# Kernel tuning notes

Hardware: AMD Instinct MI355X
Metric: run time of the kernel (lower is better)

Reference implementation:

```python
import jax, jax.numpy as jnp
import numpy as np

B, T, C = 64, 2048, 32
OUT_T = 2048

def setup_inputs() -> dict:
    key = jax.random.key(0)
    k1, k2 = jax.random.split(key)
    X = jax.random.normal(k1, (B, T, C), dtype=jnp.float32)
    # small init so deformations are modest displacements, like a trained locnet
    W_loc = jax.random.normal(k2, (T * C, OUT_T), dtype=jnp.float32) * 1e-3
    b_loc = jnp.zeros((OUT_T,), dtype=jnp.float32)
    return {"X": X, "W_loc": W_loc, "b_loc": b_loc}

def reference(X, W_loc, b_loc):
    b, t, c = X.shape
    out_t = W_loc.shape[1]
    # localization net: flatten + dense -> per-output-point displacement (B, OUT_T)
    deformation = X.reshape(b, t * c) @ W_loc + b_loc
    # sampling grid: linspace(0, T-1, OUT_T), shared across batch, shifted by deformation
    grid = jnp.linspace(0.0, jnp.float32(t - 1), out_t)  # (OUT_T,)
    x = grid[None, :] + deformation                       # (B, OUT_T) float sample coords
    # linear interpolation with clamped integer neighbors
    x0 = jnp.floor(x).astype(jnp.int32)
    x1 = x0 + 1
    x0c = jnp.clip(x0, 0, t - 1)
    x1c = jnp.clip(x1, 0, t - 1)
    batch_idx = jnp.arange(b)[:, None]                    # (B, 1)
    v0 = X[batch_idx, x0c]                                # (B, OUT_T, C) gather along T
    v1 = X[batch_idx, x1c]                                # (B, OUT_T, C)
    # weights use the CLIPPED coords cast back to float (faithful to original)
    w0 = (x1c.astype(x.dtype) - x)[..., None]             # (B, OUT_T, 1)
    w1 = (x - x0c.astype(x.dtype))[..., None]
    return w0 * v0 + w1 * v1                              # (B, OUT_T, C)
```

## Files before the change

### kernel.cpp

```cpp
#include <hip/hip_runtime.h>
#include <hip/hip_bf16.h>
#include <stdint.h>

constexpr int BATCH = 64;
constexpr int T     = 2048;
constexpr int CCH   = 32;
constexpr int OUT_T = 2048;
constexpr int K     = T * CCH;
constexpr int N     = OUT_T;

constexpr int TN     = 64;
constexpr int NBN    = N / TN;
constexpr int KSPLIT = 32;
constexpr int CK     = K / KSPLIT;
constexpr int BK     = 32;
constexpr int NS     = CK / BK;
constexpr int NWG    = NBN * KSPLIT;

typedef __attribute__((ext_vector_type(8))) short short8;
typedef __attribute__((ext_vector_type(4))) float f32x4;

__device__ __forceinline__ void split2t(float a, float b, unsigned& hpk, unsigned& lpk) {
  unsigned ua = __float_as_uint(a), ub = __float_as_uint(b);
  hpk = (ua >> 16) | (ub & 0xFFFF0000u);
  float la = a - __uint_as_float(ua & 0xFFFF0000u);
  float lb = b - __uint_as_float(ub & 0xFFFF0000u);
  __hip_bfloat162 l2 = __float22bfloat162_rn(make_float2(la, lb));
  __builtin_memcpy(&lpk, &l2, 4);
}

__global__ __launch_bounds__(256) void xsplit_kernel(
    const float* __restrict__ X, ushort* __restrict__ Xhi, ushort* __restrict__ Xlo) {
  const int i = blockIdx.x * 256 + threadIdx.x;
  const float4 v = ((const float4*)X)[i];
  unsigned h01, l01, h23, l23;
  split2t(v.x, v.y, h01, l01);
  split2t(v.z, v.w, h23, l23);
  uint2 hv; hv.x = h01; hv.y = h23;
  uint2 lv; lv.x = l01; lv.y = l23;
  ((uint2*)Xhi)[i] = hv;
  ((uint2*)Xlo)[i] = lv;
}

__global__ __launch_bounds__(256) void gemm_split_kernel(
    const ushort* __restrict__ Xhi,
    const ushort* __restrict__ Xlo,
    const float*  __restrict__ W,
    float* __restrict__ def) {
  const int bid = blockIdx.x;
  const int lb  = (bid & 7) * (NWG / 8) + (bid >> 3);
  const int bn  = lb & (NBN - 1);
  const int bk  = lb >> 5;

  const int tid  = threadIdx.x;
  const int lane = tid & 63;
  const int wave = tid >> 6;
  const int r = lane & 15;
  const int g = lane >> 4;

  __shared__ ushort Bhi[2][64][40];
  __shared__ ushort Blo[2][64][40];

  f32x4 acc[4] = {};
  const int kbase = bk * CK;

  unsigned aOff[4];
#pragma unroll
  for (int mf = 0; mf < 4; ++mf)
    aOff[mf] = (unsigned)((mf * 16 + r) * (K * 2) + (kbase + 8 * g) * 2);

  auto issueA = [&](short8 (&ah)[4], short8 (&al)[4]) {
#pragma unroll
    for (int mf = 0; mf < 4; ++mf) {
      ah[mf] = *(const short8*)((const char*)Xhi + aOff[mf]);
      al[mf] = *(const short8*)((const char*)Xlo + aOff[mf]);
    }
#pragma unroll
    for (int mf = 0; mf < 4; ++mf) aOff[mf] += BK * 2;
  };

  auto issueB = [&](int ks, float (&bb)[8]) {
    const int k0 = kbase + ks * BK;
#pragma unroll
    for (int it = 0; it < 2; ++it) {
      int flat = it * 256 + tid;
      int n  = flat & 63;
      int kq = flat >> 6;
      const float* wp = &W[(size_t)(k0 + kq * 4) * N + bn * TN + n];
#pragma unroll
      for (int j = 0; j < 4; ++j) bb[it * 4 + j] = wp[(size_t)j * N];
    }
  };

  auto stageB = [&](int buf, float (&bb)[8]) {
#pragma unroll
    for (int it = 0; it < 2; ++it) {
      int flat = it * 256 + tid;
      int n  = flat & 63;
      int kq = flat >> 6;
      unsigned h01, l01, h23, l23;
      split2t(bb[it * 4 + 0], bb[it * 4 + 1], h01, l01);
      split2t(bb[it * 4 + 2], bb[it * 4 + 3], h23, l23);
      uint2 hv; hv.x = h01; hv.y = h23;
      uint2 lv; lv.x = l01; lv.y = l23;
      *(uint2*)&Bhi[buf][n][kq * 4] = hv;
      *(uint2*)&Blo[buf][n][kq * 4] = lv;
    }
  };

  auto mfma_step = [&](int buf, short8 (&ah)[4], short8 (&al)[4]) {
    short8 bh = *(const short8*)&Bhi[buf][wave * 16 + r][g * 8];
    short8 bl = *(const short8*)&Blo[buf][wave * 16 + r][g * 8];
#pragma unroll
    for (int mf = 0; mf < 4; ++mf) {
      acc[mf] = __builtin_amdgcn_mfma_f32_16x16x32_bf16(ah[mf], bh, acc[mf], 0, 0, 0);
      acc[mf] = __builtin_amdgcn_mfma_f32_16x16x32_bf16(ah[mf], bl, acc[mf], 0, 0, 0);
      acc[mf] = __builtin_amdgcn_mfma_f32_16x16x32_bf16(al[mf], bh, acc[mf], 0, 0, 0);
    }
  };

  short8 aCh[4], aCl[4], aNh[4], aNl[4];
  float bReg0[8], bReg1[8];

  issueB(0, bReg0);
  issueB(1, bReg1);
  issueA(aCh, aCl);
  stageB(0, bReg0);
  __syncthreads();

  for (int t = 0; t < NS; t += 2) {
    issueA(aNh, aNl);
    if (t + 2 < NS) issueB(t + 2, bReg0);
    mfma_step(0, aCh, aCl);
    stageB(1, bReg1);
    __syncthreads();

    if (t + 2 < NS) issueA(aCh, aCl);
    if (t + 3 < NS) issueB(t + 3, bReg1);
    mfma_step(1, aNh, aNl);
    if (t + 2 < NS) stageB(0, bReg0);
    __syncthreads();
  }

  const int ncol = bn * TN + wave * 16 + r;
#pragma unroll
  for (int mf = 0; mf < 4; ++mf) {
    const int mbase = mf * 16 + g * 4;
#pragma unroll
    for (int q = 0; q < 4; ++q) {
      atomicAdd(&def[(size_t)(mbase + q) * N + ncol], acc[mf][q]);
    }
  }
}

__global__ __launch_bounds__(256) void resample_kernel(
    const float* __restrict__ X,
    const float* __restrict__ def,
    const float* __restrict__ b_loc,
    float* __restrict__ out) {
  const int tid = blockIdx.x * 256 + threadIdx.x;
  const int c4 = tid & 7;
  const int o  = (tid >> 3) & (OUT_T - 1);
  const int b  = tid >> 14;

  const float x = (float)o + def[b * OUT_T + o] + b_loc[o];
  const float xf = floorf(x);
  const int x0 = (int)xf;
  const int x1 = x0 + 1;
  const int x0c = min(max(x0, 0), T - 1);
  const int x1c = min(max(x1, 0), T - 1);
  const float w0 = (float)x1c - x;
  const float w1 = x - (float)x0c;

  const float4 v0 = *(const float4*)&X[((size_t)b * T + x0c) * CCH + c4 * 4];
  const float4 v1 = *(const float4*)&X[((size_t)b * T + x1c) * CCH + c4 * 4];
  float4 res;
  res.x = w0 * v0.x + w1 * v1.x;
  res.y = w0 * v0.y + w1 * v1.y;
  res.z = w0 * v0.z + w1 * v1.z;
  res.w = w0 * v0.w + w1 * v1.w;
  *(float4*)&out[((size_t)b * OUT_T + o) * CCH + c4 * 4] = res;
}

extern "C" void kernel_launch(void* const* d_in, const int* in_sizes, int n_in,
                              void* d_out, int out_size, void* d_ws, size_t ws_size,
                              hipStream_t stream) {
  const float* X     = (const float*)d_in[0];
  const float* W     = (const float*)d_in[1];
  const float* b_loc = (const float*)d_in[2];
  float* out = (float*)d_out;

  float*  def = (float*)d_ws;
  ushort* Xhi = (ushort*)((char*)d_ws + (1u << 20));
  ushort* Xlo = (ushort*)((char*)d_ws + (1u << 20) + (size_t)BATCH * K * 2);

  hipMemsetAsync(def, 0, (size_t)BATCH * N * sizeof(float), stream);

  xsplit_kernel<<<(BATCH * K / 4) / 256, 256, 0, stream>>>(X, Xhi, Xlo);

  gemm_split_kernel<<<NWG, 256, 0, stream>>>(Xhi, Xlo, W, def);

  resample_kernel<<<(BATCH * OUT_T * 8) / 256, 256, 0, stream>>>(X, def, b_loc, out);
}
```

Baseline: 863.4 us.

## Load W straight into MFMA registers and drop the LDS staging

The GEMM kernel no longer stages W through shared memory. Each lane now loads its own W column slice directly in the MFMA B-operand layout, splits it into bf16 hi/lo in registers, and keeps a four-deep register prefetch of W and A, with no __syncthreads. KSPLIT doubles to 64, giving more workgroups and a shorter K loop per workgroup, at the cost of twice as many atomicAdd reductions into def. Each W row read now covers only 64 contiguous bytes per 16 lanes, which may coalesce worse than the old 256-byte rows, and register pressure goes up.

Result: slower. 883.1 us (+2.3%).

```diff
diff --git a/kernel.cpp b/kernel.cpp
--- a/kernel.cpp
+++ b/kernel.cpp
@@ -11,7 +11,7 @@
 
 constexpr int TN     = 64;
 constexpr int NBN    = N / TN;
-constexpr int KSPLIT = 32;
+constexpr int KSPLIT = 64;
 constexpr int CK     = K / KSPLIT;
 constexpr int BK     = 32;
 constexpr int NS     = CK / BK;
@@ -42,7 +42,7 @@
   ((uint2*)Xlo)[i] = lv;
 }
 
-__global__ __launch_bounds__(256) void gemm_split_kernel(
+__global__ __launch_bounds__(256) void gemm_flat_kernel(
     const ushort* __restrict__ Xhi,
     const ushort* __restrict__ Xlo,
     const float*  __restrict__ W,
@@ -58,91 +58,57 @@
   const int r = lane & 15;
   const int g = lane >> 4;
 
-  __shared__ ushort Bhi[2][64][40];
-  __shared__ ushort Blo[2][64][40];
+  const int kbase = bk * CK;
+  const int ncol  = bn * TN + wave * 16 + r;
+
+  const float* wbase = W + (size_t)(kbase + 8 * g) * N + ncol;
 
   f32x4 acc[4] = {};
-  const int kbase = bk * CK;
+  float b0[8], b1[8], b2[8], b3[8];
+  short8 a0h[4], a0l[4], a1h[4], a1l[4];
 
-  unsigned aOff[4];
+  auto issueB = [&](int t, float (&bb)[8]) {
+    const float* p = wbase + (size_t)t * (BK * N);
 #pragma unroll
-  for (int mf = 0; mf < 4; ++mf)
-    aOff[mf] = (unsigned)((mf * 16 + r) * (K * 2) + (kbase + 8 * g) * 2);
+    for (int j = 0; j < 8; ++j) bb[j] = p[(size_t)j * N];
+  };
 
-  auto issueA = [&](short8 (&ah)[4], short8 (&al)[4]) {
+  auto issueA = [&](int t, short8 (&ah)[4], short8 (&al)[4]) {
+    const unsigned off = (unsigned)(((size_t)r * K + kbase + t * BK + 8 * g) * 2);
 #pragma unroll
     for (int mf = 0; mf < 4; ++mf) {
-      ah[mf] = *(const short8*)((const char*)Xhi + aOff[mf]);
-      al[mf] = *(const short8*)((const char*)Xlo + aOff[mf]);
-    }
-#pragma unroll
-    for (int mf = 0; mf < 4; ++mf) aOff[mf] += BK * 2;
-  };
-
-  auto issueB = [&](int ks, float (&bb)[8]) {
-    const int k0 = kbase + ks * BK;
-#pragma unroll
-    for (int it = 0; it < 2; ++it) {
-      int flat = it * 256 + tid;
-      int n  = flat & 63;
-      int kq = flat >> 6;
-      const float* wp = &W[(size_t)(k0 + kq * 4) * N + bn * TN + n];
-#pragma unroll
-      for (int j = 0; j < 4; ++j) bb[it * 4 + j] = wp[(size_t)j * N];
+      ah[mf] = *(const short8*)((const char*)Xhi + off + (size_t)mf * (16 * K * 2));
+      al[mf] = *(const short8*)((const char*)Xlo + off + (size_t)mf * (16 * K * 2));
     }
   };
 
-  auto stageB = [&](int buf, float (&bb)[8]) {
+  auto domfma = [&](float (&bb)[8], short8 (&ah)[4], short8 (&al)[4]) {
+    union { short8 s; unsigned u[4]; } bh, bl;
 #pragma unroll
-    for (int it = 0; it < 2; ++it) {
-      int flat = it * 256 + tid;
-      int n  = flat & 63;
-      int kq = flat >> 6;
-      unsigned h01, l01, h23, l23;
-      split2t(bb[it * 4 + 0], bb[it * 4 + 1], h01, l01);
-      split2t(bb[it * 4 + 2], bb[it * 4 + 3], h23, l23);
-      uint2 hv; hv.x = h01; hv.y = h23;
-      uint2 lv; lv.x = l01; lv.y = l23;
-      *(uint2*)&Bhi[buf][n][kq * 4] = hv;
-      *(uint2*)&Blo[buf][n][kq * 4] = lv;
+    for (int p2 = 0; p2 < 4; ++p2)
+      split2t(bb[2 * p2], bb[2 * p2 + 1], bh.u[p2], bl.u[p2]);
+#pragma unroll
+    for (int mf = 0; mf < 4; ++mf) {
+      acc[mf] = __builtin_amdgcn_mfma_f32_16x16x32_bf16(ah[mf], bh.s, acc[mf], 0, 0, 0);
+      acc[mf] = __builtin_amdgcn_mfma_f32_16x16x32_bf16(ah[mf], bl.s, acc[mf], 0, 0, 0);
+      acc[mf] = __builtin_amdgcn_mfma_f32_16x16x32_bf16(al[mf], bh.s, acc[mf], 0, 0, 0);
     }
   };
 
-  auto mfma_step = [&](int buf, short8 (&ah)[4], short8 (&al)[4]) {
-    short8 bh = *(const short8*)&Bhi[buf][wave * 16 + r][g * 8];
-    short8 bl = *(const short8*)&Blo[buf][wave * 16 + r][g * 8];
-#pragma unroll
-    for (int mf = 0; mf < 4; ++mf) {
-      acc[mf] = __builtin_amdgcn_mfma_f32_16x16x32_bf16(ah[mf], bh, acc[mf], 0, 0, 0);
-      acc[mf] = __builtin_amdgcn_mfma_f32_16x16x32_bf16(ah[mf], bl, acc[mf], 0, 0, 0);
-      acc[mf] = __builtin_amdgcn_mfma_f32_16x16x32_bf16(al[mf], bh, acc[mf], 0, 0, 0);
-    }
-  };
+  issueB(0, b0); issueB(1, b1); issueB(2, b2); issueB(3, b3);
+  issueA(0, a0h, a0l); issueA(1, a1h, a1l);
 
-  short8 aCh[4], aCl[4], aNh[4], aNl[4];
-  float bReg0[8], bReg1[8];
+  for (int t = 0; t < NS - 4; t += 4) {
+    domfma(b0, a0h, a0l); issueB(t + 4, b0); issueA(t + 2, a0h, a0l);
+    domfma(b1, a1h, a1l); issueB(t + 5, b1); issueA(t + 3, a1h, a1l);
+    domfma(b2, a0h, a0l); issueB(t + 6, b2); issueA(t + 4, a0h, a0l);
+    domfma(b3, a1h, a1l); issueB(t + 7, b3); issueA(t + 5, a1h, a1l);
+  }
+  domfma(b0, a0h, a0l); issueA(30, a0h, a0l);
+  domfma(b1, a1h, a1l); issueA(31, a1h, a1l);
+  domfma(b2, a0h, a0l);
+  domfma(b3, a1h, a1l);
 
-  issueB(0, bReg0);
-  issueB(1, bReg1);
-  issueA(aCh, aCl);
-  stageB(0, bReg0);
-  __syncthreads();
-
-  for (int t = 0; t < NS; t += 2) {
-    issueA(aNh, aNl);
-    if (t + 2 < NS) issueB(t + 2, bReg0);
-    mfma_step(0, aCh, aCl);
-    stageB(1, bReg1);
-    __syncthreads();
-
-    if (t + 2 < NS) issueA(aCh, aCl);
-    if (t + 3 < NS) issueB(t + 3, bReg1);
-    mfma_step(1, aNh, aNl);
-    if (t + 2 < NS) stageB(0, bReg0);
-    __syncthreads();
-  }
-
-  const int ncol = bn * TN + wave * 16 + r;
 #pragma unroll
   for (int mf = 0; mf < 4; ++mf) {
     const int mbase = mf * 16 + g * 4;
@@ -198,7 +164,7 @@
 
   xsplit_kernel<<<(BATCH * K / 4) / 256, 256, 0, stream>>>(X, Xhi, Xlo);
 
-  gemm_split_kernel<<<NWG, 256, 0, stream>>>(Xhi, Xlo, W, def);
+  gemm_flat_kernel<<<NWG, 256, 0, stream>>>(Xhi, Xlo, W, def);
 
   resample_kernel<<<(BATCH * OUT_T * 8) / 256, 256, 0, stream>>>(X, def, b_loc, out);
 }
```
